# Performance work log

Measured on AMD Instinct MI355X. Metric: run time of the kernel, lower is better.

## Reference

```python
import jax, jax.numpy as jnp
import numpy as np

B, FAN_IN, FAN_OUT, K = 4096, 4096, 4096, 65536


def setup_inputs() -> dict:
    key = jax.random.key(0)
    k1, k2, k3 = jax.random.split(key, 3)
    a = jax.random.normal(k1, (B, FAN_IN), dtype=jnp.float32)
    # hash table H(i, j) -> bucket k in [0, K); replaces the python defaultdict hh
    hash_idx = jax.random.randint(k2, (FAN_OUT, FAN_IN + 1), 0, K)
    d = FAN_OUT * (FAN_IN + 1) / K  # matches d = fan_out * fan_in / K (fan_in already +1)
    W = jax.random.normal(k3, (K,), dtype=jnp.float32) / d
    return {"a": a, "hash_idx": hash_idx, "W": W}


def reference(a, hash_idx, W):
    # append bias column of ones: a_ext [B, fan_in+1]
    ones = jnp.ones((a.shape[0], 1), dtype=a.dtype)
    a_ext = jnp.concatenate([a, ones], axis=1)
    # virtual weight matrix via hash gather: Wv[i, j] = W[H(i, j)]
    Wv = W[hash_idx]  # [fan_out, fan_in+1]
    # out[b, i] = sum_j a_ext[b, j] * W[H(i, j)]
    # identical math to: a_kj[i,b,k] = sum_{j: H(i,j)=k} a_ext[b,j]; zz = a_kj @ W; zz.T
    return jnp.einsum('bj,ij->bi', a_ext, Wv)
```

## Files before the change

### kernel.cpp

```cpp
#include <hip/hip_runtime.h>
#include <hip/hip_bf16.h>
#include <stdint.h>


#define B_DIM   4096
#define FAN_IN  4096
#define FAN_OUT 4096
#define KD      (FAN_IN + 1)
#define KP      4160

#define BM 128
#define BN 128
#define BK 32

typedef __attribute__((ext_vector_type(8))) short  short8;
typedef __attribute__((ext_vector_type(4))) float  floatx4;

__device__ __forceinline__ unsigned short f2bf(float f) {
  union { float f; unsigned u; } v; v.f = f;
  unsigned u = v.u;
  u += 0x7fffu + ((u >> 16) & 1u);
  return (unsigned short)(u >> 16);
}

__device__ __forceinline__ void async16(const void* g, void* l) {
  __builtin_amdgcn_global_load_lds(
      (const __attribute__((address_space(1))) void*)g,
      (__attribute__((address_space(3))) void*)l, 16, 0, 0);
}

__global__ __launch_bounds__(256) void build_aext(
    const float* __restrict__ a, unsigned short* __restrict__ Ae) {
  const int row = blockIdx.x;
  const float* ar = a + (size_t)row * FAN_IN;
  unsigned short* er = Ae + (size_t)row * KP;
  for (int j4 = threadIdx.x; j4 < KP / 4; j4 += 256) {
    const int j = j4 * 4;
    float x0, x1, x2, x3;
    if (j + 3 < FAN_IN) {
      const float4 v = *(const float4*)(ar + j);
      x0 = v.x; x1 = v.y; x2 = v.z; x3 = v.w;
    } else {
      x0 = (j + 0 < FAN_IN) ? ar[j + 0] : ((j + 0 == FAN_IN) ? 1.0f : 0.0f);
      x1 = (j + 1 < FAN_IN) ? ar[j + 1] : ((j + 1 == FAN_IN) ? 1.0f : 0.0f);
      x2 = (j + 2 < FAN_IN) ? ar[j + 2] : ((j + 2 == FAN_IN) ? 1.0f : 0.0f);
      x3 = (j + 3 < FAN_IN) ? ar[j + 3] : ((j + 3 == FAN_IN) ? 1.0f : 0.0f);
    }
    ushort4 o;
    o.x = f2bf(x0); o.y = f2bf(x1); o.z = f2bf(x2); o.w = f2bf(x3);
    *(ushort4*)(er + j) = o;
  }
}

__global__ __launch_bounds__(512) void build_wv(
    const int* __restrict__ hidx, const float* __restrict__ W,
    unsigned short* __restrict__ Wv) {
  __shared__ unsigned short wl[32768];
  const int t  = threadIdx.x;
  const int r0 = blockIdx.x * 4;

  int          idx[4][9];
  unsigned short res[4][9];
#pragma unroll
  for (int row = 0; row < 4; row++) {
    const int* hr = hidx + (size_t)(r0 + row) * KD;
#pragma unroll
    for (int i = 0; i < 9; i++) {
      const int j = i * 512 + t;
      idx[row][i] = (j < KD) ? hr[j] : 0;
      res[row][i] = 0;
    }
  }

  for (int h = 0; h < 2; h++) {
    __syncthreads();
    const float4* Wb = (const float4*)(W + h * 32768);
#pragma unroll
    for (int i = 0; i < 16; i++) {
      const int f4 = i * 512 + t;
      const float4 v = Wb[f4];
      ushort4 o;
      o.x = f2bf(v.x); o.y = f2bf(v.y); o.z = f2bf(v.z); o.w = f2bf(v.w);
      *(ushort4*)&wl[f4 * 4] = o;
    }
    __syncthreads();
    const int lo = h << 15;
#pragma unroll
    for (int row = 0; row < 4; row++)
#pragma unroll
      for (int i = 0; i < 9; i++) {
        const int v = idx[row][i];
        if ((v & 32768) == lo)
          res[row][i] = wl[v & 32767];
      }
  }

#pragma unroll
  for (int row = 0; row < 4; row++) {
    unsigned short* wr = Wv + (size_t)(r0 + row) * KP;
#pragma unroll
    for (int i = 0; i < 9; i++) {
      const int j = i * 512 + t;
      if (j < KD) wr[j] = res[row][i];
    }
    if (t < KP - KD) wr[KD + t] = 0;
  }
}

__global__ __launch_bounds__(256, 4) void gemm_bt(
    const unsigned short* __restrict__ A, const unsigned short* __restrict__ Bm,
    float* __restrict__ C, int M, int N) {
  __shared__ __align__(16) unsigned short As[2][BM * BK];
  __shared__ __align__(16) unsigned short Bs[2][BN * BK];

  const int tid  = threadIdx.x;
  const int lane = tid & 63;
  const int wave = tid >> 6;
  const int bm = blockIdx.y * BM;
  const int bn = blockIdx.x * BN;
  const int wm = (wave >> 1) * 64;
  const int wn = (wave & 1) * 64;
  const int q  = lane >> 4;
  const int r  = lane & 15;
  const int srow = lane >> 2;
  const int scol = (lane & 3) * 8;

  const int trow = wave * 32;
  const unsigned short* pa0 = A  + (size_t)(bm + trow      + srow) * KP + scol;
  const unsigned short* pa1 = A  + (size_t)(bm + trow + 16 + srow) * KP + scol;
  const unsigned short* pb0 = Bm + (size_t)(bn + trow      + srow) * KP + scol;
  const unsigned short* pb1 = Bm + (size_t)(bn + trow + 16 + srow) * KP + scol;
  const int l0 = trow * BK;
  const int l1 = (trow + 16) * BK;

  async16(pa0, &As[0][l0]);  async16(pa1, &As[0][l1]);
  async16(pb0, &Bs[0][l0]);  async16(pb1, &Bs[0][l1]);
  pa0 += BK; pa1 += BK; pb0 += BK; pb1 += BK;

  floatx4 acc[4][4] = {};
  int p = 0;
#pragma unroll 2
  for (int k0 = 0; k0 < KP; k0 += BK) {
    __syncthreads();
    if (k0 + BK < KP) {
      async16(pa0, &As[p ^ 1][l0]);  async16(pa1, &As[p ^ 1][l1]);
      async16(pb0, &Bs[p ^ 1][l0]);  async16(pb1, &Bs[p ^ 1][l1]);
      pa0 += BK; pa1 += BK; pb0 += BK; pb1 += BK;
    }

    short8 af[4], bf[4];
#pragma unroll
    for (int t = 0; t < 4; t++) {
      af[t] = *(const short8*)&As[p][(wm + t * 16 + r) * BK + q * 8];
      bf[t] = *(const short8*)&Bs[p][(wn + t * 16 + r) * BK + q * 8];
    }
#pragma unroll
    for (int mt = 0; mt < 4; mt++)
#pragma unroll
      for (int nt = 0; nt < 4; nt++)
        acc[mt][nt] = __builtin_amdgcn_mfma_f32_16x16x32_bf16(
            af[mt], bf[nt], acc[mt][nt], 0, 0, 0);
    p ^= 1;
  }

#pragma unroll
  for (int mt = 0; mt < 4; mt++)
#pragma unroll
    for (int nt = 0; nt < 4; nt++) {
      const int row0 = bm + wm + mt * 16 + q * 4;
      const int col  = bn + wn + nt * 16 + r;
#pragma unroll
      for (int i = 0; i < 4; i++)
        C[(size_t)(row0 + i) * N + col] = acc[mt][nt][i];
    }
}

extern "C" void kernel_launch(void* const* d_in, const int* in_sizes, int n_in,
                              void* d_out, int out_size, void* d_ws, size_t ws_size,
                              hipStream_t stream) {
  const float* a    = (const float*)d_in[0];
  const int*   hidx = (const int*)d_in[1];
  const float* W    = (const float*)d_in[2];
  float*       out  = (float*)d_out;

  unsigned short* Ae = (unsigned short*)d_ws;
  unsigned short* Wv = Ae + (size_t)B_DIM * KP;

  build_aext<<<B_DIM, 256, 0, stream>>>(a, Ae);
  build_wv<<<FAN_OUT / 4, 512, 0, stream>>>(hidx, W, Wv);
  gemm_bt<<<dim3(FAN_OUT / BN, B_DIM / BM), 256, 0, stream>>>(Ae, Wv, out, B_DIM, FAN_OUT);
}
```

Measured before the change: 340.9 us.

## Replace GEMM with 256x256 eight-wave kernel using swizzled LDS and phased pipeline

The bf16 GEMM is rewritten as a 256x256x64 tile kernel with 8 waves, 128 KB of dynamic LDS, and XOR-swizzled LDS layout to avoid bank conflicts. Each K-tile is split into four phases that interleave half-tile async global-to-LDS loads with MFMA batches, using s_setprio and explicit barriers/waitcnt. The aim is more data reuse per byte loaded and better overlap of memory traffic with matrix math. The costs are higher register and LDS pressure, only 256 blocks for the GPU's CUs, and fragile hand-written synchronisation.

```diff
diff --git a/kernel.cpp b/kernel.cpp
--- a/kernel.cpp
+++ b/kernel.cpp
@@ -8,10 +8,11 @@
 #define FAN_OUT 4096
 #define KD      (FAN_IN + 1)
 #define KP      4160
-
-#define BM 128
-#define BN 128
-#define BK 32
+#define NKT     65
+
+#define BM 256
+#define BN 256
+#define BK 64
 
 typedef __attribute__((ext_vector_type(8))) short  short8;
 typedef __attribute__((ext_vector_type(4))) float  floatx4;
@@ -107,71 +108,161 @@
   }
 }
 
-__global__ __launch_bounds__(256, 4) void gemm_bt(
+
+#define STAGE_A(buf, h, ts)                                                        \
+  do {                                                                             \
+    async16(pa + ((h) * 128 + 0)  * KP + (ts) * 64,                                \
+            smb + ((buf) << 15) + ((h) << 14) + dA);                               \
+    async16(pa + ((h) * 128 + 64) * KP + (ts) * 64,                                \
+            smb + ((buf) << 15) + ((h) << 14) + 8192 + dA);                        \
+  } while (0)
+
+#define STAGE_B(buf, h, ts)                                                        \
+  do {                                                                             \
+    async16(pb + ((h) * 128 + 0)  * KP + (ts) * 64,                                \
+            smb + 65536 + ((buf) << 15) + ((h) << 14) + dA);                       \
+    async16(pb + ((h) * 128 + 64) * KP + (ts) * 64,                                \
+            smb + 65536 + ((buf) << 15) + ((h) << 14) + 8192 + dA);                \
+  } while (0)
+
+#define PHASE_MID()                                                                \
+  do {                                                                             \
+    asm volatile("" ::: "memory");                                                 \
+    __builtin_amdgcn_s_barrier();                                                  \
+    asm volatile("s_waitcnt lgkmcnt(0)" ::: "memory");                             \
+    __builtin_amdgcn_sched_barrier(0);                                             \
+    __builtin_amdgcn_s_setprio(1);                                                 \
+  } while (0)
+
+#define PHASE_END()                                                                \
+  do {                                                                             \
+    __builtin_amdgcn_s_setprio(0);                                                 \
+    asm volatile("" ::: "memory");                                                 \
+    __builtin_amdgcn_s_barrier();                                                  \
+    asm volatile("" ::: "memory");                                                 \
+  } while (0)
+
+#define PHASE_END_TILE()                                                           \
+  do {                                                                             \
+    __builtin_amdgcn_s_setprio(0);                                                 \
+    asm volatile("s_waitcnt vmcnt(4)" ::: "memory");                               \
+    __builtin_amdgcn_s_barrier();                                                  \
+    asm volatile("" ::: "memory");                                                 \
+  } while (0)
+
+#define MFMA2(ACC, AF, BF)                                                         \
+  do {                                                                             \
+    ACC = __builtin_amdgcn_mfma_f32_16x16x32_bf16((AF)[0], (BF)[0], ACC, 0, 0, 0); \
+    ACC = __builtin_amdgcn_mfma_f32_16x16x32_bf16((AF)[1], (BF)[1], ACC, 0, 0, 0); \
+  } while (0)
+
+__global__ __launch_bounds__(512, 2) void gemm_bt8(
     const unsigned short* __restrict__ A, const unsigned short* __restrict__ Bm,
     float* __restrict__ C, int M, int N) {
-  __shared__ __align__(16) unsigned short As[2][BM * BK];
-  __shared__ __align__(16) unsigned short Bs[2][BN * BK];
-
-  const int tid  = threadIdx.x;
-  const int lane = tid & 63;
-  const int wave = tid >> 6;
-  const int bm = blockIdx.y * BM;
-  const int bn = blockIdx.x * BN;
-  const int wm = (wave >> 1) * 64;
-  const int wn = (wave & 1) * 64;
-  const int q  = lane >> 4;
-  const int r  = lane & 15;
-  const int srow = lane >> 2;
-  const int scol = (lane & 3) * 8;
-
-  const int trow = wave * 32;
-  const unsigned short* pa0 = A  + (size_t)(bm + trow      + srow) * KP + scol;
-  const unsigned short* pa1 = A  + (size_t)(bm + trow + 16 + srow) * KP + scol;
-  const unsigned short* pb0 = Bm + (size_t)(bn + trow      + srow) * KP + scol;
-  const unsigned short* pb1 = Bm + (size_t)(bn + trow + 16 + srow) * KP + scol;
-  const int l0 = trow * BK;
-  const int l1 = (trow + 16) * BK;
-
-  async16(pa0, &As[0][l0]);  async16(pa1, &As[0][l1]);
-  async16(pb0, &Bs[0][l0]);  async16(pb1, &Bs[0][l1]);
-  pa0 += BK; pa1 += BK; pb0 += BK; pb1 += BK;
-
-  floatx4 acc[4][4] = {};
-  int p = 0;
-#pragma unroll 2
-  for (int k0 = 0; k0 < KP; k0 += BK) {
-    __syncthreads();
-    if (k0 + BK < KP) {
-      async16(pa0, &As[p ^ 1][l0]);  async16(pa1, &As[p ^ 1][l1]);
-      async16(pb0, &Bs[p ^ 1][l0]);  async16(pb1, &Bs[p ^ 1][l1]);
-      pa0 += BK; pa1 += BK; pb0 += BK; pb1 += BK;
-    }
-
-    short8 af[4], bf[4];
-#pragma unroll
-    for (int t = 0; t < 4; t++) {
-      af[t] = *(const short8*)&As[p][(wm + t * 16 + r) * BK + q * 8];
-      bf[t] = *(const short8*)&Bs[p][(wn + t * 16 + r) * BK + q * 8];
-    }
-#pragma unroll
-    for (int mt = 0; mt < 4; mt++)
-#pragma unroll
-      for (int nt = 0; nt < 4; nt++)
-        acc[mt][nt] = __builtin_amdgcn_mfma_f32_16x16x32_bf16(
-            af[mt], bf[nt], acc[mt][nt], 0, 0, 0);
-    p ^= 1;
-  }
-
-#pragma unroll
-  for (int mt = 0; mt < 4; mt++)
-#pragma unroll
-    for (int nt = 0; nt < 4; nt++) {
-      const int row0 = bm + wm + mt * 16 + q * 4;
-      const int col  = bn + wn + nt * 16 + r;
-#pragma unroll
-      for (int i = 0; i < 4; i++)
-        C[(size_t)(row0 + i) * N + col] = acc[mt][nt][i];
+  extern __shared__ char smb[];
+  const int tid = threadIdx.x;
+  const int l   = tid & 63;
+  const int w   = tid >> 6;
+  const int wm  = w >> 2;
+  const int wn  = w & 3;
+  const int bm  = blockIdx.y * BM;
+  const int bn  = blockIdx.x * BN;
+  const int q   = l >> 4;
+  const int r   = l & 15;
+
+  const int lrow = l >> 3;
+  const int lcol = ((l & 7) ^ lrow) * 8;
+  const unsigned short* pa = A  + (size_t)(bm + w * 8 + lrow) * KP + lcol;
+  const unsigned short* pb = Bm + (size_t)(bn + w * 8 + lrow) * KP + lcol;
+  const int dA = w * 1024;
+
+  const int abase = r * 128 + ((q ^ (r & 7)) << 4);
+
+  floatx4 acc[8][4] = {};
+
+  STAGE_A(0, 0, 0); STAGE_A(0, 1, 0);
+  STAGE_B(0, 0, 0); STAGE_B(0, 1, 0);
+  STAGE_B(1, 0, 1); STAGE_A(1, 0, 1);
+  asm volatile("s_waitcnt vmcnt(4)" ::: "memory");
+  __builtin_amdgcn_s_barrier();
+  asm volatile("" ::: "memory");
+
+#pragma unroll 1
+  for (int t = 0; t < NKT; ++t) {
+    const int p   = t & 1;
+    const int ts1 = (t + 1 < NKT) ? t + 1 : NKT - 1;
+    const int ts2 = (t + 2 < NKT) ? t + 2 : NKT - 1;
+    const int ar  = (p << 15) + (wm << 14);
+    const int br  = 65536 + (p << 15) + ((wn >> 1) << 14) + ((wn & 1) << 13);
+
+    short8 af[4][2], bf[4][2];
+
+#pragma unroll
+    for (int mi = 0; mi < 4; ++mi) {
+      af[mi][0] = *(const short8*)(smb + ar + mi * 2048 + abase);
+      af[mi][1] = *(const short8*)(smb + ar + mi * 2048 + (abase ^ 64));
+    }
+#pragma unroll
+    for (int ni = 0; ni < 2; ++ni) {
+      bf[ni][0] = *(const short8*)(smb + br + ni * 2048 + abase);
+      bf[ni][1] = *(const short8*)(smb + br + ni * 2048 + (abase ^ 64));
+    }
+    STAGE_A(p ^ 1, 1, ts1);
+    PHASE_MID();
+#pragma unroll
+    for (int mi = 0; mi < 4; ++mi)
+#pragma unroll
+      for (int ni = 0; ni < 2; ++ni) MFMA2(acc[mi][ni], af[mi], bf[ni]);
+    PHASE_END();
+
+#pragma unroll
+    for (int ni = 2; ni < 4; ++ni) {
+      bf[ni][0] = *(const short8*)(smb + br + ni * 2048 + abase);
+      bf[ni][1] = *(const short8*)(smb + br + ni * 2048 + (abase ^ 64));
+    }
+    STAGE_B(p ^ 1, 1, ts1);
+    PHASE_MID();
+#pragma unroll
+    for (int mi = 0; mi < 4; ++mi)
+#pragma unroll
+      for (int ni = 2; ni < 4; ++ni) MFMA2(acc[mi][ni], af[mi], bf[ni]);
+    PHASE_END();
+
+#pragma unroll
+    for (int mi = 0; mi < 4; ++mi) {
+      af[mi][0] = *(const short8*)(smb + ar + (mi + 4) * 2048 + abase);
+      af[mi][1] = *(const short8*)(smb + ar + (mi + 4) * 2048 + (abase ^ 64));
+    }
+    STAGE_B(p, 0, ts2);
+    PHASE_MID();
+#pragma unroll
+    for (int mi = 0; mi < 4; ++mi)
+#pragma unroll
+      for (int ni = 0; ni < 2; ++ni) MFMA2(acc[mi + 4][ni], af[mi], bf[ni]);
+    PHASE_END();
+
+    STAGE_A(p, 0, ts2);
+    PHASE_MID();
+#pragma unroll
+    for (int mi = 0; mi < 4; ++mi)
+#pragma unroll
+      for (int ni = 2; ni < 4; ++ni) MFMA2(acc[mi + 4][ni], af[mi], bf[ni]);
+    PHASE_END_TILE();
+  }
+
+  asm volatile("s_waitcnt vmcnt(0)" ::: "memory");
+
+  const int r0 = bm + wm * 128;
+  const int c0 = bn + wn * 64;
+#pragma unroll
+  for (int mi = 0; mi < 8; ++mi)
+#pragma unroll
+    for (int ni = 0; ni < 4; ++ni) {
+      const int row0 = r0 + mi * 16 + q * 4;
+      const int col  = c0 + ni * 16 + r;
+#pragma unroll
+      for (int i = 0; i < 4; ++i)
+        C[(size_t)(row0 + i) * N + col] = acc[mi][ni][i];
     }
 }
 
@@ -186,7 +277,14 @@
   unsigned short* Ae = (unsigned short*)d_ws;
   unsigned short* Wv = Ae + (size_t)B_DIM * KP;
 
+  static bool attr_set = false;
+  if (!attr_set) {
+    hipFuncSetAttribute((const void*)gemm_bt8,
+                        hipFuncAttributeMaxDynamicSharedMemorySize, 131072);
+    attr_set = true;
+  }
+
   build_aext<<<B_DIM, 256, 0, stream>>>(a, Ae);
   build_wv<<<FAN_OUT / 4, 512, 0, stream>>>(hidx, W, Wv);
-  gemm_bt<<<dim3(FAN_OUT / BN, B_DIM / BM), 256, 0, stream>>>(Ae, Wv, out, B_DIM, FAN_OUT);
-}
+  gemm_bt8<<<dim3(FAN_OUT / BN, B_DIM / BM), 512, 131072, stream>>>(Ae, Wv, out, B_DIM, FAN_OUT);
+}
```

Result: faster. 300.0 us (-12.0%).
